# Performance work log

Hardware: AMD Instinct MI355X
Metric: run time of the kernel (lower is better)

## Reference

```python
import jax, jax.numpy as jnp
import numpy as np

B = 64      # graphs per batch
N = 1024    # nodes per graph (equal-size graphs -> static top-k)
D = 256     # in_dim
DEG = 16    # avg degree
K = 512     # k = ratio * N, ratio = 0.5
E = B * N * DEG
NT = B * N


def setup_inputs() -> dict:
    key = jax.random.key(0)
    ks = jax.random.split(key, 8)
    feature = jax.random.normal(ks[0], (NT, D), jnp.float32)
    gid = jnp.repeat(jnp.arange(B), N * DEG)          # graph id per edge
    src = gid * N + jax.random.randint(ks[1], (E,), 0, N)
    dst = gid * N + jax.random.randint(ks[2], (E,), 0, N)
    label = jax.random.randint(ks[3], (B,), 0, 2)
    W = jax.random.normal(ks[4], (D, 1), jnp.float32) / np.sqrt(D)   # GraphConv weight
    b = jnp.zeros((1,), jnp.float32)                                  # GraphConv bias
    lin1_w = jax.random.normal(ks[5], (2, 1), jnp.float32) / np.sqrt(2.0)
    lin1_b = jnp.zeros((1,), jnp.float32)
    return dict(feature=feature, src=src, dst=dst, label=label,
                W=W, b=b, lin1_w=lin1_w, lin1_b=lin1_b)


def reference(feature, src, dst, label, W, b, lin1_w, lin1_b):
    fdt = feature.dtype
    # ---- get_bias_score: distance-to-class-center score ----
    node_label = jnp.repeat(label, N).astype(fdt)                 # [NT]
    gemb = feature.reshape(B, N, D).mean(axis=1)                  # AvgPooling per graph [B, D]
    lab_f = label.astype(fdt)                                     # [B]
    n1 = jnp.maximum(lab_f.sum(), 1.0)
    n0 = jnp.maximum((1.0 - lab_f).sum(), 1.0)
    center0 = (gemb * (1.0 - lab_f)[:, None]).sum(0) / n0         # [D]
    center1 = (gemb * lab_f[:, None]).sum(0) / n1                 # [D]
    d0 = jnp.sqrt(((feature - center0) ** 2).sum(-1))             # [NT]
    d1 = jnp.sqrt(((feature - center1) ** 2).sum(-1))             # [NT]
    score_distance = (d0 - d1) * ((node_label - 0.5) * 2.0)       # [NT]
    # ---- GraphConv(in_dim, 1), norm='both' (DGL semantics) ----
    ones_e = jnp.ones((E,), fdt)
    deg_out = jax.ops.segment_sum(ones_e, src, NT)
    deg_in = jax.ops.segment_sum(ones_e, dst, NT)
    ns = jnp.maximum(deg_out, 1.0) ** -0.5                        # src-side norm
    nd = jnp.maximum(deg_in, 1.0) ** -0.5                         # dst-side norm
    h = (feature @ W) * ns[:, None]                               # project first (out<in) [NT,1]
    agg = jax.ops.segment_sum(h[src], dst, NT)                    # [NT,1]
    score_gcn = (agg * nd[:, None] + b)[:, 0]                     # [NT]
    # ---- combine two scores with lin1: Linear(2, 1) ----
    score = jnp.stack([score_gcn, score_distance], axis=-1) @ lin1_w + lin1_b  # [NT,1]
    sflat = score[:, 0]
    # ---- per-graph top-k (mytopk with equal-size graphs -> static k) ----
    _, idx = jax.lax.top_k(sflat.reshape(B, N), K)                # [B,K] local indices
    perm = (idx + (jnp.arange(B) * N)[:, None]).reshape(-1)       # [B*K] global indices
    mask = jnp.ones((NT,), bool).at[perm].set(False)
    perm_com = jnp.nonzero(mask, size=NT - B * K)[0]              # complement, static size
    # ---- gather + tanh-gated features ----
    feature_dis = feature[perm] * jnp.tanh(sflat[perm])[:, None]          # [B*K, D]
    feature_com = feature[perm_com] * jnp.tanh(sflat[perm_com])[:, None]  # [B*(N-K), D]
    score_soft = jax.nn.softmax(score, axis=0)                    # softmax over all nodes
    return feature_dis, feature_com, perm, perm_com, score_soft
```

## Files before the change

### kernel.cpp

```cpp
#include <hip/hip_runtime.h>
#include <math.h>

#define Bg   64
#define Nn   1024
#define Dd   256
#define Ee   (Bg * Nn * 16)
#define EPG  16384
#define EPB  4096
#define NT   (Bg * Nn)
#define Kk   512

#define OFF_DIS   0
#define OFF_COM   8388608
#define OFF_PERM  16777216
#define OFF_PCOM  16809984
#define OFF_SOFT  16842752

#define WS_H0      0
#define WS_SFLAT   (NT * 4)
#define WS_GPART   (NT * 4 * 2)
#define WS_C0      (WS_GPART + 512 * 256 * 4)
#define WS_C1      (WS_C0 + 1024)
#define WS_REDM    (WS_C1 + 1024)
#define WS_REDS    (WS_REDM + 256)
#define WS_PERMI   (WS_REDS + 256)
#define WS_PCOMI   (WS_PERMI + 32768 * 4)
#define WS_EPACK   (WS_PCOMI + 32768 * 4)
#define WS_DO4     (WS_EPACK + Ee * 4)
#define WS_DI4     (WS_DO4 + 4 * NT * 4)
#define WS_AGG4    (WS_DI4 + 4 * NT * 4)

__global__ __launch_bounds__(256) void k_mix(
        const float* __restrict__ f, const float* __restrict__ W,
        const int* __restrict__ src, const int* __restrict__ dst,
        float* __restrict__ gpart, float* __restrict__ h0,
        unsigned* __restrict__ epack, int* __restrict__ do4, int* __restrict__ di4) {
    __shared__ int smem[2048];
    int blk = blockIdx.x;
    int t   = threadIdx.x;
    if (blk < 512) {
        float* scol = (float*)smem;
        int base = blk * 128;
        int lane = t & 63, wid = t >> 6;
        const float4* f4 = (const float4*)f;
        const float4* W4 = (const float4*)W;
        float4 w = W4[lane];
        float4 cs = make_float4(0.f, 0.f, 0.f, 0.f);
        for (int r = 0; r < 32; ++r) {
            int row = base + wid * 32 + r;
            float4 v = f4[(size_t)row * 64 + lane];
            cs.x += v.x; cs.y += v.y; cs.z += v.z; cs.w += v.w;
            float d = v.x * w.x + v.y * w.y + v.z * w.z + v.w * w.w;
            for (int o = 32; o > 0; o >>= 1) d += __shfl_xor(d, o);
            if (lane == 0) h0[row] = d;
        }
        ((float4*)scol)[wid * 64 + lane] = cs;
        __syncthreads();
        float s = scol[t] + scol[Dd + t] + scol[2 * Dd + t] + scol[3 * Dd + t];
        gpart[blk * Dd + t] = s;
    } else {
        int* sdo = smem;
        int* sdi = smem + 1024;
        int blk2 = blk - 512;
        int g = blk2 >> 2, sl = blk2 & 3;
        #pragma unroll
        for (int j = 0; j < 4; ++j) { sdo[t + j * 256] = 0; sdi[t + j * 256] = 0; }
        __syncthreads();
        int ebase = g * EPG + sl * EPB;
        const int4* s4 = (const int4*)(src + ebase);
        const int4* d4 = (const int4*)(dst + ebase);
        uint4* p4 = (uint4*)(epack + ebase);
        #pragma unroll
        for (int i = t; i < EPB / 4; i += 256) {
            int4 ss = s4[i];
            int4 dd = d4[i];
            int s0 = ss.x & (Nn - 1), s1 = ss.y & (Nn - 1), s2 = ss.z & (Nn - 1), s3 = ss.w & (Nn - 1);
            int e0 = dd.x & (Nn - 1), e1 = dd.y & (Nn - 1), e2 = dd.z & (Nn - 1), e3 = dd.w & (Nn - 1);
            uint4 pk;
            pk.x = (unsigned)(s0 | (e0 << 16));
            pk.y = (unsigned)(s1 | (e1 << 16));
            pk.z = (unsigned)(s2 | (e2 << 16));
            pk.w = (unsigned)(s3 | (e3 << 16));
            p4[i] = pk;
            atomicAdd(&sdo[s0], 1); atomicAdd(&sdo[s1], 1);
            atomicAdd(&sdo[s2], 1); atomicAdd(&sdo[s3], 1);
            atomicAdd(&sdi[e0], 1); atomicAdd(&sdi[e1], 1);
            atomicAdd(&sdi[e2], 1); atomicAdd(&sdi[e3], 1);
        }
        __syncthreads();
        int base = sl * NT + g * Nn;
        #pragma unroll
        for (int j = 0; j < 4; ++j) {
            do4[base + t + j * 256] = sdo[t + j * 256];
            di4[base + t + j * 256] = sdi[t + j * 256];
        }
    }
}

__global__ __launch_bounds__(1024) void k_edgeB(
        const unsigned* __restrict__ epack, const float* __restrict__ h0,
        const int* __restrict__ do4, const float* __restrict__ gpart,
        const int* __restrict__ label, float* __restrict__ agg4,
        float* __restrict__ c0, float* __restrict__ c1) {
    __shared__ float shn[Nn];
    __shared__ float sagg[Nn];
    int blk = blockIdx.x, t = threadIdx.x;
    int g = blk >> 2, sl = blk & 3;
    {
        int idx = g * Nn + t;
        int dg = do4[idx] + do4[NT + idx] + do4[2 * NT + idx] + do4[3 * NT + idx];
        if (dg < 1) dg = 1;
        shn[t] = h0[idx] / sqrtf((float)dg);
        sagg[t] = 0.f;
    }
    __syncthreads();
    {
        const uint4* p4 = (const uint4*)(epack + g * EPG + sl * EPB);
        uint4 pk = p4[t];
        atomicAdd(&sagg[pk.x >> 16], shn[pk.x & 0xFFFF]);
        atomicAdd(&sagg[pk.y >> 16], shn[pk.y & 0xFFFF]);
        atomicAdd(&sagg[pk.z >> 16], shn[pk.z & 0xFFFF]);
        atomicAdd(&sagg[pk.w >> 16], shn[pk.w & 0xFFFF]);
    }
    __syncthreads();
    agg4[sl * NT + g * Nn + t] = sagg[t];
    if (blk == 0 && t < Dd) {
        int n1 = 0;
        for (int gg = 0; gg < Bg; ++gg) n1 += label[gg];
        float fn1 = fmaxf((float)n1, 1.f);
        float fn0 = fmaxf((float)(Bg - n1), 1.f);
        float s0 = 0.f, s1 = 0.f;
        for (int gg = 0; gg < Bg; ++gg) {
            float v = 0.f;
            for (int p = 0; p < 8; ++p) v += gpart[(gg * 8 + p) * Dd + t];
            v *= (1.f / (float)Nn);
            if (label[gg]) s1 += v; else s0 += v;
        }
        c0[t] = s0 / fn0;
        c1[t] = s1 / fn1;
    }
}

__global__ void k_score(const float* __restrict__ f, const float* __restrict__ c0,
                        const float* __restrict__ c1, const float* __restrict__ agg4,
                        const int* __restrict__ di4, const int* __restrict__ label,
                        const float* __restrict__ b, const float* __restrict__ lw,
                        const float* __restrict__ lb, float* __restrict__ sflat) {
    int node = blockIdx.x * 4 + (threadIdx.x >> 6);
    int lane = threadIdx.x & 63;
    const float4* f4  = (const float4*)f;
    const float4* c04 = (const float4*)c0;
    const float4* c14 = (const float4*)c1;
    float4 v = f4[(size_t)node * 64 + lane];
    float4 a = c04[lane];
    float4 bb = c14[lane];
    float dx, acc0, acc1;
    dx = v.x - a.x;  acc0  = dx * dx;
    dx = v.y - a.y;  acc0 += dx * dx;
    dx = v.z - a.z;  acc0 += dx * dx;
    dx = v.w - a.w;  acc0 += dx * dx;
    dx = v.x - bb.x; acc1  = dx * dx;
    dx = v.y - bb.y; acc1 += dx * dx;
    dx = v.z - bb.z; acc1 += dx * dx;
    dx = v.w - bb.w; acc1 += dx * dx;
    for (int o = 32; o > 0; o >>= 1) {
        acc0 += __shfl_xor(acc0, o);
        acc1 += __shfl_xor(acc1, o);
    }
    if (lane == 0) {
        float d0 = sqrtf(acc0), d1 = sqrtf(acc1);
        int g = node >> 10;
        float sgn = label[g] ? 1.f : -1.f;
        float sdist = (d0 - d1) * sgn;
        float agg = agg4[node] + agg4[NT + node] + agg4[2 * NT + node] + agg4[3 * NT + node];
        int dg = di4[node] + di4[NT + node] + di4[2 * NT + node] + di4[3 * NT + node];
        if (dg < 1) dg = 1;
        float sgcn = agg / sqrtf((float)dg) + b[0];
        sflat[node] = sgcn * lw[0] + sdist * lw[1] + lb[0];
    }
}

__global__ __launch_bounds__(512) void k_topk(
        const float* __restrict__ sflat, int* __restrict__ permI,
        int* __restrict__ pcomI, float* __restrict__ out,
        float* __restrict__ redM, float* __restrict__ redS) {
    __shared__ unsigned long long sk[1024];
    __shared__ int   sflag[1024];
    __shared__ int   swave[8];
    __shared__ float sred[16];
    int g = blockIdx.x, t = threadIdx.x;
    int lane = t & 63, w = t >> 6;
    float v0 = sflat[g * Nn + t];
    float v1 = sflat[g * Nn + t + 512];
    unsigned u0 = __float_as_uint(v0);
    unsigned u1 = __float_as_uint(v1);
    unsigned o0 = u0 ^ ((u0 >> 31) ? 0xFFFFFFFFu : 0x80000000u);
    unsigned o1 = u1 ^ ((u1 >> 31) ? 0xFFFFFFFFu : 0x80000000u);
    sk[t]       = ((unsigned long long)o0 << 32) | (unsigned)(1023 - t);
    sk[t + 512] = ((unsigned long long)o1 << 32) | (unsigned)(1023 - (t + 512));
    __syncthreads();
    for (int k = 2; k <= 1024; k <<= 1) {
        for (int j = k >> 1; j > 0; j >>= 1) {
            int l = ((t & ~(j - 1)) << 1) | (t & (j - 1));
            int r = l | j;
            unsigned long long a = sk[l], bk = sk[r];
            bool up = ((l & k) == 0);
            if ((a < bk) == up) { sk[l] = bk; sk[r] = a; }
            __syncthreads();
        }
    }
    sflag[t] = 1; sflag[t + 512] = 1;
    __syncthreads();
    {
        int loc = 1023 - (int)(sk[t] & 0xFFFFFFFFu);
        sflag[loc] = 0;
        int gi = g * Nn + loc;
        permI[g * Kk + t] = gi;
        out[OFF_PERM + g * Kk + t] = (float)gi;
    }
    __syncthreads();
    int f0 = sflag[2 * t], f1 = sflag[2 * t + 1];
    int f2 = f0 + f1;
    int inc = f2;
    for (int o = 1; o < 64; o <<= 1) {
        int y = __shfl_up(inc, o);
        if (lane >= o) inc += y;
    }
    if (lane == 63) swave[w] = inc;
    __syncthreads();
    if (t < 8) {
        int a = swave[t];
        for (int o = 1; o < 8; o <<= 1) {
            int y = __shfl_up(a, o);
            if (t >= o) a += y;
        }
        swave[t] = a;
    }
    __syncthreads();
    int basep = ((w > 0) ? swave[w - 1] : 0) + (inc - f2);
    if (f0) {
        int gi = g * Nn + 2 * t;
        pcomI[g * Kk + basep] = gi;
        out[OFF_PCOM + g * Kk + basep] = (float)gi;
    }
    if (f1) {
        int pos = basep + f0;
        int gi = g * Nn + 2 * t + 1;
        pcomI[g * Kk + pos] = gi;
        out[OFF_PCOM + g * Kk + pos] = (float)gi;
    }
    float m = fmaxf(v0, v1);
    for (int o = 32; o > 0; o >>= 1) m = fmaxf(m, __shfl_xor(m, o));
    if (lane == 0) sred[w] = m;
    __syncthreads();
    if (t < 8) {
        float a = sred[t];
        for (int o = 4; o > 0; o >>= 1) a = fmaxf(a, __shfl_xor(a, o));
        if (t == 0) sred[0] = a;
    }
    __syncthreads();
    m = sred[0];
    float s = expf(v0 - m) + expf(v1 - m);
    for (int o = 32; o > 0; o >>= 1) s += __shfl_xor(s, o);
    if (lane == 0) sred[8 + w] = s;
    __syncthreads();
    if (t < 8) {
        float a = sred[8 + t];
        for (int o = 4; o > 0; o >>= 1) a += __shfl_xor(a, o);
        if (t == 0) { redM[g] = m; redS[g] = a; }
    }
}

__global__ void k_write(const float* __restrict__ f, const int* __restrict__ permI,
                        const int* __restrict__ pcomI, const float* __restrict__ sflat,
                        const float* __restrict__ redM, const float* __restrict__ redS,
                        float* __restrict__ out) {
    __shared__ float sMS[2];
    int t = threadIdx.x;
    if (t < 64) {
        float m = redM[t];
        float mm = m;
        for (int o = 32; o > 0; o >>= 1) mm = fmaxf(mm, __shfl_xor(mm, o));
        float s = redS[t] * expf(m - mm);
        for (int o = 32; o > 0; o >>= 1) s += __shfl_xor(s, o);
        if (t == 0) { sMS[0] = mm; sMS[1] = s; }
    }
    __syncthreads();
    float M = sMS[0], S = sMS[1];
    if (t < 4) {
        int i = blockIdx.x * 4 + t;
        out[OFF_SOFT + i] = expf(sflat[i] - M) / S;
    }
    int j = blockIdx.x * 4 + (t >> 6);
    int lane = t & 63;
    int row = (j < 32768) ? permI[j] : pcomI[j - 32768];
    float tv = tanhf(sflat[row]);
    const float4* f4 = (const float4*)f;
    float4* o4 = (float4*)out;
    float4 v = f4[(size_t)row * 64 + lane];
    o4[(size_t)j * 64 + lane] = make_float4(v.x * tv, v.y * tv, v.z * tv, v.w * tv);
}

extern "C" void kernel_launch(void* const* d_in, const int* in_sizes, int n_in,
                              void* d_out, int out_size, void* d_ws, size_t ws_size,
                              hipStream_t stream) {
    const float* feature = (const float*)d_in[0];
    const int*   src     = (const int*)d_in[1];
    const int*   dst     = (const int*)d_in[2];
    const int*   label   = (const int*)d_in[3];
    const float* W       = (const float*)d_in[4];
    const float* b       = (const float*)d_in[5];
    const float* lw      = (const float*)d_in[6];
    const float* lb      = (const float*)d_in[7];
    float* out = (float*)d_out;
    char*  ws  = (char*)d_ws;

    float*    h0    = (float*)(ws + WS_H0);
    float*    sflat = (float*)(ws + WS_SFLAT);
    float*    gpart = (float*)(ws + WS_GPART);
    float*    c0    = (float*)(ws + WS_C0);
    float*    c1    = (float*)(ws + WS_C1);
    float*    redM  = (float*)(ws + WS_REDM);
    float*    redS  = (float*)(ws + WS_REDS);
    int*      permI = (int*)(ws + WS_PERMI);
    int*      pcomI = (int*)(ws + WS_PCOMI);
    unsigned* epack = (unsigned*)(ws + WS_EPACK);
    int*      do4   = (int*)(ws + WS_DO4);
    int*      di4   = (int*)(ws + WS_DI4);
    float*    agg4  = (float*)(ws + WS_AGG4);

    k_mix<<<768, 256, 0, stream>>>(feature, W, src, dst, gpart, h0, epack, do4, di4);
    k_edgeB<<<256, 1024, 0, stream>>>(epack, h0, do4, gpart, label, agg4, c0, c1);
    k_score<<<NT / 4, 256, 0, stream>>>(feature, c0, c1, agg4, di4, label, b, lw, lb, sflat);
    k_topk<<<Bg, 512, 0, stream>>>(sflat, permI, pcomI, out, redM, redS);
    k_write<<<NT / 4, 256, 0, stream>>>(feature, permI, pcomI, sflat, redM, redS, out);
}
```

Measured before the change: 208.3 us.

## Fuse degree, aggregation, scoring and top-k into one per-graph kernel

Replaces four kernels with a column-sum/projection kernel plus a single per-graph kernel. The per-graph kernel keeps packed edges, degrees, GCN aggregation, class centers, distance scores, bitonic top-k and softmax partials in shared memory. This removes global intermediates (packed edges, per-slice degree and aggregation buffers) and two kernel launches. The cost is parallelism: the feature distance pass now runs on only 64 blocks, one per graph, which may underuse memory bandwidth.

Result: slower. 214.7 us (+3.1%).

```diff
diff --git a/kernel.cpp b/kernel.cpp
--- a/kernel.cpp
+++ b/kernel.cpp
@@ -4,9 +4,7 @@
 #define Bg   64
 #define Nn   1024
 #define Dd   256
-#define Ee   (Bg * Nn * 16)
 #define EPG  16384
-#define EPB  4096
 #define NT   (Bg * Nn)
 #define Kk   512
 
@@ -16,62 +14,72 @@
 #define OFF_PCOM  16809984
 #define OFF_SOFT  16842752
 
-#define WS_H0      0
-#define WS_SFLAT   (NT * 4)
-#define WS_GPART   (NT * 4 * 2)
-#define WS_C0      (WS_GPART + 512 * 256 * 4)
-#define WS_C1      (WS_C0 + 1024)
-#define WS_REDM    (WS_C1 + 1024)
-#define WS_REDS    (WS_REDM + 256)
-#define WS_PERMI   (WS_REDS + 256)
-#define WS_PCOMI   (WS_PERMI + 32768 * 4)
-#define WS_EPACK   (WS_PCOMI + 32768 * 4)
-#define WS_DO4     (WS_EPACK + Ee * 4)
-#define WS_DI4     (WS_DO4 + 4 * NT * 4)
-#define WS_AGG4    (WS_DI4 + 4 * NT * 4)
-
-__global__ __launch_bounds__(256) void k_mix(
+#define WS_H0     0
+#define WS_SFLAT  (NT * 4)
+#define WS_GPART  (NT * 4 * 2)
+#define WS_REDM   (WS_GPART + 512 * 256 * 4)
+#define WS_REDS   (WS_REDM + 256)
+#define WS_PERMI  (WS_REDS + 256)
+#define WS_PCOMI  (WS_PERMI + 32768 * 4)
+
+__global__ __launch_bounds__(256) void k_col(
         const float* __restrict__ f, const float* __restrict__ W,
-        const int* __restrict__ src, const int* __restrict__ dst,
-        float* __restrict__ gpart, float* __restrict__ h0,
-        unsigned* __restrict__ epack, int* __restrict__ do4, int* __restrict__ di4) {
-    __shared__ int smem[2048];
-    int blk = blockIdx.x;
-    int t   = threadIdx.x;
-    if (blk < 512) {
-        float* scol = (float*)smem;
-        int base = blk * 128;
-        int lane = t & 63, wid = t >> 6;
-        const float4* f4 = (const float4*)f;
-        const float4* W4 = (const float4*)W;
-        float4 w = W4[lane];
-        float4 cs = make_float4(0.f, 0.f, 0.f, 0.f);
-        for (int r = 0; r < 32; ++r) {
-            int row = base + wid * 32 + r;
-            float4 v = f4[(size_t)row * 64 + lane];
-            cs.x += v.x; cs.y += v.y; cs.z += v.z; cs.w += v.w;
-            float d = v.x * w.x + v.y * w.y + v.z * w.z + v.w * w.w;
-            for (int o = 32; o > 0; o >>= 1) d += __shfl_xor(d, o);
-            if (lane == 0) h0[row] = d;
-        }
-        ((float4*)scol)[wid * 64 + lane] = cs;
-        __syncthreads();
-        float s = scol[t] + scol[Dd + t] + scol[2 * Dd + t] + scol[3 * Dd + t];
-        gpart[blk * Dd + t] = s;
-    } else {
-        int* sdo = smem;
-        int* sdi = smem + 1024;
-        int blk2 = blk - 512;
-        int g = blk2 >> 2, sl = blk2 & 3;
+        float* __restrict__ gpart, float* __restrict__ h0) {
+    __shared__ float scol[1024];
+    int blk = blockIdx.x, t = threadIdx.x;
+    int base = blk * 128;
+    int lane = t & 63, wid = t >> 6;
+    const float4* f4 = (const float4*)f;
+    const float4* W4 = (const float4*)W;
+    float4 w = W4[lane];
+    float4 cs = make_float4(0.f, 0.f, 0.f, 0.f);
+    for (int r = 0; r < 32; ++r) {
+        int row = base + wid * 32 + r;
+        float4 v = f4[(size_t)row * 64 + lane];
+        cs.x += v.x; cs.y += v.y; cs.z += v.z; cs.w += v.w;
+        float d = v.x * w.x + v.y * w.y + v.z * w.z + v.w * w.w;
+        for (int o = 32; o > 0; o >>= 1) d += __shfl_xor(d, o);
+        if (lane == 0) h0[row] = d;
+    }
+    ((float4*)scol)[wid * 64 + lane] = cs;
+    __syncthreads();
+    gpart[blk * Dd + t] = scol[t] + scol[Dd + t] + scol[2 * Dd + t] + scol[3 * Dd + t];
+}
+
+__global__ __launch_bounds__(1024) void k_graph(
+        const float* __restrict__ f, const int* __restrict__ src,
+        const int* __restrict__ dst, const int* __restrict__ label,
+        const float* __restrict__ h0, const float* __restrict__ gpart,
+        const float* __restrict__ b, const float* __restrict__ lw,
+        const float* __restrict__ lb, float* __restrict__ sflat,
+        int* __restrict__ permI, int* __restrict__ pcomI,
+        float* __restrict__ out, float* __restrict__ redM, float* __restrict__ redS) {
+    __shared__ uint4 ep4[4096];
+    __shared__ int   sdo[1024];
+    __shared__ int   sdi[1024];
+    __shared__ float shn[1024];
+    __shared__ float ssc[1024];
+    __shared__ float sc0[1024];
+    __shared__ float sc1[1024];
+    __shared__ float c0f[256];
+    __shared__ float c1f[256];
+    __shared__ float sfl[1024];
+    __shared__ unsigned long long sk[1024];
+    __shared__ int   sflag[1024];
+    __shared__ int   swave[8];
+    __shared__ float sred[33];
+
+    int g = blockIdx.x, t = threadIdx.x;
+    int lane = t & 63, w16 = t >> 6;
+
+    sdo[t] = 0; sdi[t] = 0;
+    __syncthreads();
+
+    {
+        const int4* s4 = (const int4*)(src + g * EPG);
+        const int4* d4 = (const int4*)(dst + g * EPG);
         #pragma unroll
-        for (int j = 0; j < 4; ++j) { sdo[t + j * 256] = 0; sdi[t + j * 256] = 0; }
-        __syncthreads();
-        int ebase = g * EPG + sl * EPB;
-        const int4* s4 = (const int4*)(src + ebase);
-        const int4* d4 = (const int4*)(dst + ebase);
-        uint4* p4 = (uint4*)(epack + ebase);
-        #pragma unroll
-        for (int i = t; i < EPB / 4; i += 256) {
+        for (int i = t; i < EPG / 4; i += 1024) {
             int4 ss = s4[i];
             int4 dd = d4[i];
             int s0 = ss.x & (Nn - 1), s1 = ss.y & (Nn - 1), s2 = ss.z & (Nn - 1), s3 = ss.w & (Nn - 1);
@@ -81,137 +89,122 @@
             pk.y = (unsigned)(s1 | (e1 << 16));
             pk.z = (unsigned)(s2 | (e2 << 16));
             pk.w = (unsigned)(s3 | (e3 << 16));
-            p4[i] = pk;
+            ep4[i] = pk;
             atomicAdd(&sdo[s0], 1); atomicAdd(&sdo[s1], 1);
             atomicAdd(&sdo[s2], 1); atomicAdd(&sdo[s3], 1);
             atomicAdd(&sdi[e0], 1); atomicAdd(&sdi[e1], 1);
             atomicAdd(&sdi[e2], 1); atomicAdd(&sdi[e3], 1);
         }
-        __syncthreads();
-        int base = sl * NT + g * Nn;
-        #pragma unroll
-        for (int j = 0; j < 4; ++j) {
-            do4[base + t + j * 256] = sdo[t + j * 256];
-            di4[base + t + j * 256] = sdi[t + j * 256];
-        }
-    }
-}
-
-__global__ __launch_bounds__(1024) void k_edgeB(
-        const unsigned* __restrict__ epack, const float* __restrict__ h0,
-        const int* __restrict__ do4, const float* __restrict__ gpart,
-        const int* __restrict__ label, float* __restrict__ agg4,
-        float* __restrict__ c0, float* __restrict__ c1) {
-    __shared__ float shn[Nn];
-    __shared__ float sagg[Nn];
-    int blk = blockIdx.x, t = threadIdx.x;
-    int g = blk >> 2, sl = blk & 3;
-    {
-        int idx = g * Nn + t;
-        int dg = do4[idx] + do4[NT + idx] + do4[2 * NT + idx] + do4[3 * NT + idx];
-        if (dg < 1) dg = 1;
-        shn[t] = h0[idx] / sqrtf((float)dg);
-        sagg[t] = 0.f;
-    }
-    __syncthreads();
-    {
-        const uint4* p4 = (const uint4*)(epack + g * EPG + sl * EPB);
-        uint4 pk = p4[t];
-        atomicAdd(&sagg[pk.x >> 16], shn[pk.x & 0xFFFF]);
-        atomicAdd(&sagg[pk.y >> 16], shn[pk.y & 0xFFFF]);
-        atomicAdd(&sagg[pk.z >> 16], shn[pk.z & 0xFFFF]);
-        atomicAdd(&sagg[pk.w >> 16], shn[pk.w & 0xFFFF]);
-    }
-    __syncthreads();
-    agg4[sl * NT + g * Nn + t] = sagg[t];
-    if (blk == 0 && t < Dd) {
+    }
+    __syncthreads();
+
+    {
+        int dg = sdo[t]; if (dg < 1) dg = 1;
+        shn[t] = h0[g * Nn + t] / sqrtf((float)dg);
+        ssc[t] = 0.f;
+    }
+    __syncthreads();
+
+    #pragma unroll
+    for (int i = t; i < EPG / 4; i += 1024) {
+        uint4 pk = ep4[i];
+        atomicAdd(&ssc[pk.x >> 16], shn[pk.x & 0xFFFF]);
+        atomicAdd(&ssc[pk.y >> 16], shn[pk.y & 0xFFFF]);
+        atomicAdd(&ssc[pk.z >> 16], shn[pk.z & 0xFFFF]);
+        atomicAdd(&ssc[pk.w >> 16], shn[pk.w & 0xFFFF]);
+    }
+    __syncthreads();
+
+    {
+        int dg = sdi[t]; if (dg < 1) dg = 1;
+        ssc[t] = ssc[t] / sqrtf((float)dg) + b[0];
+        int col = t & 255, chunk = t >> 8;
+        float a0 = 0.f, a1 = 0.f;
+        for (int gg = chunk * 16; gg < chunk * 16 + 16; ++gg) {
+            float v = 0.f;
+            #pragma unroll
+            for (int p = 0; p < 8; ++p) v += gpart[(gg * 8 + p) * Dd + col];
+            if (label[gg]) a1 += v; else a0 += v;
+        }
+        sc0[t] = a0; sc1[t] = a1;
+    }
+    __syncthreads();
+    if (t < Dd) {
         int n1 = 0;
         for (int gg = 0; gg < Bg; ++gg) n1 += label[gg];
         float fn1 = fmaxf((float)n1, 1.f);
         float fn0 = fmaxf((float)(Bg - n1), 1.f);
-        float s0 = 0.f, s1 = 0.f;
-        for (int gg = 0; gg < Bg; ++gg) {
-            float v = 0.f;
-            for (int p = 0; p < 8; ++p) v += gpart[(gg * 8 + p) * Dd + t];
-            v *= (1.f / (float)Nn);
-            if (label[gg]) s1 += v; else s0 += v;
-        }
-        c0[t] = s0 / fn0;
-        c1[t] = s1 / fn1;
-    }
-}
-
-__global__ void k_score(const float* __restrict__ f, const float* __restrict__ c0,
-                        const float* __restrict__ c1, const float* __restrict__ agg4,
-                        const int* __restrict__ di4, const int* __restrict__ label,
-                        const float* __restrict__ b, const float* __restrict__ lw,
-                        const float* __restrict__ lb, float* __restrict__ sflat) {
-    int node = blockIdx.x * 4 + (threadIdx.x >> 6);
-    int lane = threadIdx.x & 63;
-    const float4* f4  = (const float4*)f;
-    const float4* c04 = (const float4*)c0;
-    const float4* c14 = (const float4*)c1;
-    float4 v = f4[(size_t)node * 64 + lane];
-    float4 a = c04[lane];
-    float4 bb = c14[lane];
-    float dx, acc0, acc1;
-    dx = v.x - a.x;  acc0  = dx * dx;
-    dx = v.y - a.y;  acc0 += dx * dx;
-    dx = v.z - a.z;  acc0 += dx * dx;
-    dx = v.w - a.w;  acc0 += dx * dx;
-    dx = v.x - bb.x; acc1  = dx * dx;
-    dx = v.y - bb.y; acc1 += dx * dx;
-    dx = v.z - bb.z; acc1 += dx * dx;
-    dx = v.w - bb.w; acc1 += dx * dx;
-    for (int o = 32; o > 0; o >>= 1) {
-        acc0 += __shfl_xor(acc0, o);
-        acc1 += __shfl_xor(acc1, o);
-    }
-    if (lane == 0) {
-        float d0 = sqrtf(acc0), d1 = sqrtf(acc1);
-        int g = node >> 10;
+        float s0 = sc0[t] + sc0[256 + t] + sc0[512 + t] + sc0[768 + t];
+        float s1 = sc1[t] + sc1[256 + t] + sc1[512 + t] + sc1[768 + t];
+        c0f[t] = s0 * (1.f / (float)Nn) / fn0;
+        c1f[t] = s1 * (1.f / (float)Nn) / fn1;
+    }
+    __syncthreads();
+
+    {
+        int rg = lane >> 4, sub = lane & 15;
+        float4 c0r[4], c1r[4];
+        #pragma unroll
+        for (int it = 0; it < 4; ++it) {
+            c0r[it] = ((const float4*)c0f)[it * 16 + sub];
+            c1r[it] = ((const float4*)c1f)[it * 16 + sub];
+        }
+        float lw0 = lw[0], lw1 = lw[1], lb0 = lb[0];
         float sgn = label[g] ? 1.f : -1.f;
-        float sdist = (d0 - d1) * sgn;
-        float agg = agg4[node] + agg4[NT + node] + agg4[2 * NT + node] + agg4[3 * NT + node];
-        int dg = di4[node] + di4[NT + node] + di4[2 * NT + node] + di4[3 * NT + node];
-        if (dg < 1) dg = 1;
-        float sgcn = agg / sqrtf((float)dg) + b[0];
-        sflat[node] = sgcn * lw[0] + sdist * lw[1] + lb[0];
-    }
-}
-
-__global__ __launch_bounds__(512) void k_topk(
-        const float* __restrict__ sflat, int* __restrict__ permI,
-        int* __restrict__ pcomI, float* __restrict__ out,
-        float* __restrict__ redM, float* __restrict__ redS) {
-    __shared__ unsigned long long sk[1024];
-    __shared__ int   sflag[1024];
-    __shared__ int   swave[8];
-    __shared__ float sred[16];
-    int g = blockIdx.x, t = threadIdx.x;
-    int lane = t & 63, w = t >> 6;
-    float v0 = sflat[g * Nn + t];
-    float v1 = sflat[g * Nn + t + 512];
-    unsigned u0 = __float_as_uint(v0);
-    unsigned u1 = __float_as_uint(v1);
-    unsigned o0 = u0 ^ ((u0 >> 31) ? 0xFFFFFFFFu : 0x80000000u);
-    unsigned o1 = u1 ^ ((u1 >> 31) ? 0xFFFFFFFFu : 0x80000000u);
-    sk[t]       = ((unsigned long long)o0 << 32) | (unsigned)(1023 - t);
-    sk[t + 512] = ((unsigned long long)o1 << 32) | (unsigned)(1023 - (t + 512));
+        const float4* f4 = (const float4*)f;
+        for (int grp = 0; grp < 16; ++grp) {
+            int row = w16 * 64 + grp * 4 + rg;
+            size_t bofs = (size_t)(g * Nn + row) * 64;
+            float a0 = 0.f, a1 = 0.f;
+            #pragma unroll
+            for (int it = 0; it < 4; ++it) {
+                float4 v = f4[bofs + it * 16 + sub];
+                float dx;
+                dx = v.x - c0r[it].x; a0 += dx * dx;
+                dx = v.y - c0r[it].y; a0 += dx * dx;
+                dx = v.z - c0r[it].z; a0 += dx * dx;
+                dx = v.w - c0r[it].w; a0 += dx * dx;
+                dx = v.x - c1r[it].x; a1 += dx * dx;
+                dx = v.y - c1r[it].y; a1 += dx * dx;
+                dx = v.z - c1r[it].z; a1 += dx * dx;
+                dx = v.w - c1r[it].w; a1 += dx * dx;
+            }
+            #pragma unroll
+            for (int o = 1; o < 16; o <<= 1) {
+                a0 += __shfl_xor(a0, o);
+                a1 += __shfl_xor(a1, o);
+            }
+            if (sub == 0) {
+                float sdist = (sqrtf(a0) - sqrtf(a1)) * sgn;
+                float val = ssc[row] * lw0 + sdist * lw1 + lb0;
+                sfl[row] = val;
+                sflat[g * Nn + row] = val;
+            }
+        }
+    }
+    __syncthreads();
+
+    {
+        unsigned u = __float_as_uint(sfl[t]);
+        unsigned ox = u ^ ((u >> 31) ? 0xFFFFFFFFu : 0x80000000u);
+        sk[t] = ((unsigned long long)ox << 32) | (unsigned)(1023 - t);
+    }
     __syncthreads();
     for (int k = 2; k <= 1024; k <<= 1) {
         for (int j = k >> 1; j > 0; j >>= 1) {
-            int l = ((t & ~(j - 1)) << 1) | (t & (j - 1));
-            int r = l | j;
-            unsigned long long a = sk[l], bk = sk[r];
-            bool up = ((l & k) == 0);
-            if ((a < bk) == up) { sk[l] = bk; sk[r] = a; }
+            if (t < 512) {
+                int l = ((t & ~(j - 1)) << 1) | (t & (j - 1));
+                int r = l | j;
+                unsigned long long A = sk[l], Bk = sk[r];
+                bool up = ((l & k) == 0);
+                if ((A < Bk) == up) { sk[l] = Bk; sk[r] = A; }
+            }
             __syncthreads();
         }
     }
-    sflag[t] = 1; sflag[t + 512] = 1;
-    __syncthreads();
-    {
+    sflag[t] = 1;
+    __syncthreads();
+    if (t < 512) {
         int loc = 1023 - (int)(sk[t] & 0xFFFFFFFFu);
         sflag[loc] = 0;
         int gi = g * Nn + loc;
@@ -219,14 +212,16 @@
         out[OFF_PERM + g * Kk + t] = (float)gi;
     }
     __syncthreads();
-    int f0 = sflag[2 * t], f1 = sflag[2 * t + 1];
-    int f2 = f0 + f1;
-    int inc = f2;
-    for (int o = 1; o < 64; o <<= 1) {
-        int y = __shfl_up(inc, o);
-        if (lane >= o) inc += y;
-    }
-    if (lane == 63) swave[w] = inc;
+    int f0 = 0, f1 = 0, f2 = 0, inc = 0;
+    if (t < 512) {
+        f0 = sflag[2 * t]; f1 = sflag[2 * t + 1];
+        f2 = f0 + f1; inc = f2;
+        for (int o = 1; o < 64; o <<= 1) {
+            int y = __shfl_up(inc, o);
+            if (lane >= o) inc += y;
+        }
+        if (lane == 63) swave[w16] = inc;
+    }
     __syncthreads();
     if (t < 8) {
         int a = swave[t];
@@ -237,37 +232,40 @@
         swave[t] = a;
     }
     __syncthreads();
-    int basep = ((w > 0) ? swave[w - 1] : 0) + (inc - f2);
-    if (f0) {
-        int gi = g * Nn + 2 * t;
-        pcomI[g * Kk + basep] = gi;
-        out[OFF_PCOM + g * Kk + basep] = (float)gi;
-    }
-    if (f1) {
-        int pos = basep + f0;
-        int gi = g * Nn + 2 * t + 1;
-        pcomI[g * Kk + pos] = gi;
-        out[OFF_PCOM + g * Kk + pos] = (float)gi;
-    }
-    float m = fmaxf(v0, v1);
+    if (t < 512) {
+        int basep = ((w16 > 0) ? swave[w16 - 1] : 0) + (inc - f2);
+        if (f0) {
+            int gi = g * Nn + 2 * t;
+            pcomI[g * Kk + basep] = gi;
+            out[OFF_PCOM + g * Kk + basep] = (float)gi;
+        }
+        if (f1) {
+            int pos = basep + f0;
+            int gi = g * Nn + 2 * t + 1;
+            pcomI[g * Kk + pos] = gi;
+            out[OFF_PCOM + g * Kk + pos] = (float)gi;
+        }
+    }
+    float v = sfl[t];
+    float m = v;
     for (int o = 32; o > 0; o >>= 1) m = fmaxf(m, __shfl_xor(m, o));
-    if (lane == 0) sred[w] = m;
-    __syncthreads();
-    if (t < 8) {
+    if (lane == 0) sred[w16] = m;
+    __syncthreads();
+    if (t < 16) {
         float a = sred[t];
-        for (int o = 4; o > 0; o >>= 1) a = fmaxf(a, __shfl_xor(a, o));
-        if (t == 0) sred[0] = a;
-    }
-    __syncthreads();
-    m = sred[0];
-    float s = expf(v0 - m) + expf(v1 - m);
+        for (int o = 8; o > 0; o >>= 1) a = fmaxf(a, __shfl_xor(a, o));
+        if (t == 0) sred[32] = a;
+    }
+    __syncthreads();
+    float M = sred[32];
+    float s = expf(v - M);
     for (int o = 32; o > 0; o >>= 1) s += __shfl_xor(s, o);
-    if (lane == 0) sred[8 + w] = s;
-    __syncthreads();
-    if (t < 8) {
-        float a = sred[8 + t];
-        for (int o = 4; o > 0; o >>= 1) a += __shfl_xor(a, o);
-        if (t == 0) { redM[g] = m; redS[g] = a; }
+    if (lane == 0) sred[16 + w16] = s;
+    __syncthreads();
+    if (t < 16) {
+        float a = sred[16 + t];
+        for (int o = 8; o > 0; o >>= 1) a += __shfl_xor(a, o);
+        if (t == 0) { redM[g] = M; redS[g] = a; }
     }
 }
 
@@ -315,23 +313,16 @@
     float* out = (float*)d_out;
     char*  ws  = (char*)d_ws;
 
-    float*    h0    = (float*)(ws + WS_H0);
-    float*    sflat = (float*)(ws + WS_SFLAT);
-    float*    gpart = (float*)(ws + WS_GPART);
-    float*    c0    = (float*)(ws + WS_C0);
-    float*    c1    = (float*)(ws + WS_C1);
-    float*    redM  = (float*)(ws + WS_REDM);
-    float*    redS  = (float*)(ws + WS_REDS);
-    int*      permI = (int*)(ws + WS_PERMI);
-    int*      pcomI = (int*)(ws + WS_PCOMI);
-    unsigned* epack = (unsigned*)(ws + WS_EPACK);
-    int*      do4   = (int*)(ws + WS_DO4);
-    int*      di4   = (int*)(ws + WS_DI4);
-    float*    agg4  = (float*)(ws + WS_AGG4);
-
-    k_mix<<<768, 256, 0, stream>>>(feature, W, src, dst, gpart, h0, epack, do4, di4);
-    k_edgeB<<<256, 1024, 0, stream>>>(epack, h0, do4, gpart, label, agg4, c0, c1);
-    k_score<<<NT / 4, 256, 0, stream>>>(feature, c0, c1, agg4, di4, label, b, lw, lb, sflat);
-    k_topk<<<Bg, 512, 0, stream>>>(sflat, permI, pcomI, out, redM, redS);
-    k_write<<<NT / 4, 256, 0, stream>>>(feature, permI, pcomI, sflat, redM, redS, out);
+    float* h0    = (float*)(ws + WS_H0);
+    float* sflat = (float*)(ws + WS_SFLAT);
+    float* gpart = (float*)(ws + WS_GPART);
+    float* redM  = (float*)(ws + WS_REDM);
+    float* redS  = (float*)(ws + WS_REDS);
+    int*   permI = (int*)(ws + WS_PERMI);
+    int*   pcomI = (int*)(ws + WS_PCOMI);
+
+    k_col  <<<512,    256,  0, stream>>>(feature, W, gpart, h0);
+    k_graph<<<Bg,     1024, 0, stream>>>(feature, src, dst, label, h0, gpart,
+                                         b, lw, lb, sflat, permI, pcomI, out, redM, redS);
+    k_write<<<NT / 4, 256,  0, stream>>>(feature, permI, pcomI, sflat, redM, redS, out);
 }
```
